# Optimization experiments

Measured on AMD Instinct MI355X. Metric: run time of the kernel, lower is better.

Reference implementation:

```python
import jax, jax.numpy as jnp
import numpy as np

EPS = 1.55e-5  # tf.math.l2_normalize epsilon semantics: x / sqrt(max(sum(x^2), eps))


def _l2norm_tokens(t):
    # normalize over the token axis (-2), matching tf.math.l2_normalize(axis=-2)
    sq = jnp.sum(t * t, axis=-2, keepdims=True)
    return t * jax.lax.rsqrt(jnp.maximum(sq, EPS))


def setup_inputs() -> dict:
    key = jax.random.key(0)
    ks = jax.random.split(key, 4)
    B, H, W, C = 16, 64, 64, 512
    heads = 8
    return {
        "x": jax.random.normal(ks[0], (B, H, W, C), jnp.float32),
        "qkv_w": jax.random.normal(ks[1], (C, 3 * C), jnp.float32) * (C ** -0.5),
        "q_bias": jnp.zeros((C,), jnp.float32),
        "v_bias": jnp.zeros((C,), jnp.float32),
        "scale": jnp.ones((heads, 1, 1), jnp.float32),
        "proj_w": jax.random.normal(ks[2], (C, C), jnp.float32) * (C ** -0.5),
        "proj_b": jnp.zeros((C,), jnp.float32),
    }


def reference(x, qkv_w, q_bias, v_bias, scale, proj_w, proj_b):
    B, H, W, C = x.shape
    heads = scale.shape[0]
    d = C // heads
    N = H * W

    # 1x1 conv QKV (no conv bias) + concatenated [q_bias, 0, v_bias]
    qkv = jnp.einsum("bhwc,cf->bhwf", x, qkv_w)
    qkv = qkv + jnp.concatenate([q_bias, jnp.zeros_like(q_bias), v_bias])
    # [B, N, heads, 3, d] -> [B, heads, N, 3, d]
    qkv = qkv.reshape(B, N, heads, 3, d).transpose(0, 2, 1, 3, 4)
    q, k, v = qkv[..., 0, :], qkv[..., 1, :], qkv[..., 2, :]  # each [B, heads, N, d]

    q = _l2norm_tokens(q)
    k = _l2norm_tokens(k)

    # channel-attention: [B, heads, d, d]
    attn = jnp.einsum("bhnd,bhne->bhde", q * jnp.exp(scale), k)
    attn = jax.nn.softmax(attn, axis=-1)

    # matmul(attn, v^T) -> [B, heads, d, N]; perm [0,3,1,2] -> [B, N, heads, d]
    out = jnp.einsum("bhde,bhne->bhdn", attn, v)
    out = out.transpose(0, 3, 1, 2).reshape(B, H, W, C)

    # output 1x1 conv projection with bias
    return jnp.einsum("bhwc,cf->bhwf", out, proj_w) + proj_b
```

## Files before the change

kernel.cpp:

```cpp
#include <hip/hip_runtime.h>
#include <stdint.h>
#include <stddef.h>

#define BATCH  16
#define HEADS  8
#define NTOK   4096
#define CDIM   512
#define FDIM   1536

typedef short bf16x8 __attribute__((ext_vector_type(8)));
typedef float fx4    __attribute__((ext_vector_type(4)));

__device__ __forceinline__ uint16_t f2bf(float f) {
    uint32_t u = __float_as_uint(f);
    return (uint16_t)((u + 0x7FFFu + ((u >> 16) & 1u)) >> 16);
}
__device__ __forceinline__ float bf2f(uint16_t u) {
    return __uint_as_float(((uint32_t)u) << 16);
}
__device__ __forceinline__ void gload16(const uint16_t* g, uint16_t* l) {
    __builtin_amdgcn_global_load_lds(
        (const __attribute__((address_space(1))) uint32_t*)(g),
        (__attribute__((address_space(3))) uint32_t*)(l), 16, 0, 0);
}

__global__ void transpose_w_kernel(const float* __restrict__ qkv_w,
                                   const float* __restrict__ proj_w,
                                   uint16_t* __restrict__ Wt,
                                   uint16_t* __restrict__ Pt) {
    __shared__ uint16_t tile[32][33];
    int blk = blockIdx.x;
    const float* src; uint16_t* dst; int W, Hh, r0, c0;
    if (blk < 768) {
        int tr = blk / 48, tc = blk % 48;
        src = qkv_w; dst = Wt; W = 1536; Hh = 512; r0 = tr * 32; c0 = tc * 32;
    } else {
        blk -= 768;
        int tr = blk / 16, tc = blk % 16;
        src = proj_w; dst = Pt; W = 512; Hh = 512; r0 = tr * 32; c0 = tc * 32;
    }
    const int tx = threadIdx.x & 31, ty = threadIdx.x >> 5;
    #pragma unroll
    for (int j = 0; j < 4; j++)
        tile[ty + 8 * j][tx] = f2bf(src[(size_t)(r0 + ty + 8 * j) * W + c0 + tx]);
    __syncthreads();
    #pragma unroll
    for (int j = 0; j < 4; j++)
        dst[(size_t)(c0 + ty + 8 * j) * Hh + r0 + tx] = tile[tx][ty + 8 * j];
}

__global__ void prep_kernel(const float* __restrict__ X,
                            uint16_t* __restrict__ Xb,
                            float* __restrict__ Sqk) {
    const int tid = blockIdx.x * blockDim.x + threadIdx.x;
    const int stride = gridDim.x * blockDim.x;
    for (int i = tid; i < (1 << 22); i += stride) {
        const fx4* src = reinterpret_cast<const fx4*>(X + (size_t)i * 8);
        fx4 v0 = src[0], v1 = src[1];
        union { bf16x8 v; uint16_t u[8]; } pk;
        #pragma unroll
        for (int e = 0; e < 4; e++) { pk.u[e] = f2bf(v0[e]); pk.u[4 + e] = f2bf(v1[e]); }
        reinterpret_cast<bf16x8*>(Xb)[i] = pk.v;
    }
    for (int i = tid; i < 16384; i += stride) Sqk[i] = 0.0f;
}

__global__ __launch_bounds__(256) void gemm_qkv_kernel(
        const uint16_t* __restrict__ Xb, const uint16_t* __restrict__ Wt,
        const float* __restrict__ q_bias, const float* __restrict__ v_bias,
        uint16_t* __restrict__ QT, uint16_t* __restrict__ KT,
        uint16_t* __restrict__ VT,
        float* __restrict__ Sq, float* __restrict__ Sk) {
    __shared__ uint16_t ring[3][8192];
    const int bx = blockIdx.x;
    const int swz = (bx & 7) * 768 + (bx >> 3);
    const int tm = swz / 12, tn = swz % 12;
    const int gm = tm * 128, gn = tn * 128;
    const int b = gm >> 12, tok0 = gm & 4095;
    const int t = threadIdx.x, lane = t & 63, w = t >> 6;
    const int wm = w >> 1, wn = w & 1;
    const int l15 = lane & 15, lg = lane >> 4;
    fx4 acc[4][4] = {};
    const int srow = t >> 2;
    const int scol = (((t & 3) ^ (srow & 3)) << 3);
    const uint16_t* gA = Xb + (size_t)(gm + srow) * 512 + scol;
    const uint16_t* gB = Wt + (size_t)(gn + srow) * 512 + scol;
    auto stage = [&](int kt_) {
        const int s_ = kt_ % 3;
        const int k0_ = kt_ * 32;
        gload16(gA + k0_,                    &ring[s_][t * 8]);
        gload16(gA + (size_t)64 * 512 + k0_, &ring[s_][t * 8 + 2048]);
        gload16(gB + k0_,                    &ring[s_][4096 + t * 8]);
        gload16(gB + (size_t)64 * 512 + k0_, &ring[s_][4096 + t * 8 + 2048]);
    };
    stage(0); stage(1);
    #pragma unroll
    for (int kt = 0; kt < 16; ++kt) {
        if (kt < 15) asm volatile("s_waitcnt vmcnt(4) lgkmcnt(0)" ::: "memory");
        else         asm volatile("s_waitcnt vmcnt(0) lgkmcnt(0)" ::: "memory");
        __builtin_amdgcn_s_barrier();
        if (kt < 14) stage(kt + 2);
        const uint16_t* As = &ring[kt % 3][0];
        const uint16_t* Bs = &ring[kt % 3][4096];
        bf16x8 af[4], bfr[4];
        #pragma unroll
        for (int m = 0; m < 4; m++) {
            const int row = wm * 64 + m * 16 + l15;
            af[m] = *reinterpret_cast<const bf16x8*>(&As[row * 32 + ((lg ^ (row & 3)) << 3)]);
        }
        #pragma unroll
        for (int n = 0; n < 4; n++) {
            const int row = wn * 64 + n * 16 + l15;
            bfr[n] = *reinterpret_cast<const bf16x8*>(&Bs[row * 32 + ((lg ^ (row & 3)) << 3)]);
        }
        __builtin_amdgcn_s_setprio(1);
        #pragma unroll
        for (int m = 0; m < 4; m++)
            #pragma unroll
            for (int n = 0; n < 4; n++)
                acc[m][n] = __builtin_amdgcn_mfma_f32_16x16x32_bf16(
                    af[m], bfr[n], acc[m][n], 0, 0, 0);
        __builtin_amdgcn_s_setprio(0);
    }
    __syncthreads();
    const int u = (gn >> 6) + wn;
    const int type = u % 3;
    const int h = u / 3;
    const int bh = b * 8 + h;
    float biasn[4];
    #pragma unroll
    for (int n = 0; n < 4; n++) {
        const int col = gn + wn * 64 + n * 16 + l15;
        biasn[n] = (col < 512) ? q_bias[col]
                  : ((col < 1024) ? 0.0f : v_bias[col - 1024]);
    }
    if (type < 2) {
        uint16_t* T = (type == 0) ? QT : KT;
        #pragma unroll
        for (int n = 0; n < 4; n++) {
            const int d = n * 16 + l15;
            uint16_t* dst = T + ((size_t)bh * 64 + d) * 4096 + tok0 + wm * 64 + lg * 4;
            float ss = 0.f;
            #pragma unroll
            for (int m = 0; m < 4; m++) {
                union { uint16_t u4[4]; uint64_t q; } pk;
                #pragma unroll
                for (int r = 0; r < 4; r++) {
                    const float f = acc[m][n][r] + biasn[n];
                    pk.u4[r] = f2bf(f);
                    ss += f * f;
                }
                *reinterpret_cast<uint64_t*>(dst + m * 16) = pk.q;
            }
            ss += __shfl_xor(ss, 16, 64);
            ss += __shfl_xor(ss, 32, 64);
            if (lg == 0)
                atomicAdd((type == 0 ? Sq : Sk) + bh * 64 + d, ss);
        }
    } else {
        uint16_t* vs = &ring[0][0];
        #pragma unroll
        for (int n = 0; n < 4; n++) {
            const int lcol = n * 16 + l15;
            #pragma unroll
            for (int m = 0; m < 4; m++)
                #pragma unroll
                for (int r = 0; r < 4; r++) {
                    const int lrow = wm * 64 + m * 16 + lg * 4 + r;
                    vs[lrow * 64 + (lcol ^ ((lrow & 7) << 3))] =
                        f2bf(acc[m][n][r] + biasn[n]);
                }
        }
    }
    __syncthreads();
    {
        const int u0 = gn >> 6;
        const int uv = (u0 % 3 == 2) ? u0 : (((u0 + 1) % 3 == 2) ? (u0 + 1) : -1);
        if (uv >= 0) {
            const uint16_t* vs = &ring[0][0];
            const int hv = uv / 3;
            const int row = t >> 1, c0v = (t & 1) * 32;
            uint16_t* dst = VT + (size_t)(gm + row) * 512 + hv * 64 + c0v;
            #pragma unroll
            for (int cc = 0; cc < 4; cc++) {
                const int col = c0v + cc * 8;
                bf16x8 vv = *reinterpret_cast<const bf16x8*>(
                    &vs[row * 64 + (col ^ ((row & 7) << 3))]);
                *reinterpret_cast<bf16x8*>(dst + cc * 8) = vv;
            }
        }
    }
}

__global__ __launch_bounds__(256) void attn_qk_kernel(
        const uint16_t* __restrict__ QT, const uint16_t* __restrict__ KT,
        float* __restrict__ Gpart) {
    __shared__ uint16_t Qs[2][8192];
    __shared__ uint16_t Ks[2][8192];
    const int blk = blockIdx.x;
    const int bh = blk >> 2, quarter = blk & 3;
    const int t = threadIdx.x, lane = t & 63, w = t >> 6;
    const int l15 = lane & 15, lg = lane >> 4;
    const int wr = w >> 1, wc = w & 1;
    fx4 acc[2][2] = {};
    const uint16_t* qbase = QT + (size_t)bh * 64 * 4096;
    const uint16_t* kbase = KT + (size_t)bh * 64 * 4096;
    auto stage = [&](int it_) {
        const int tokt = quarter * 1024 + it_ * 128;
        uint16_t* qd = &Qs[it_ & 1][0];
        uint16_t* kd = &Ks[it_ & 1][0];
        #pragma unroll
        for (int j = 0; j < 4; j++) {
            const int li = j * 256 + t;
            const int row = li >> 4;
            const int src_off = (((li & 15) ^ (row & 7)) << 3);
            gload16(qbase + (size_t)row * 4096 + tokt + src_off, qd + li * 8);
            gload16(kbase + (size_t)row * 4096 + tokt + src_off, kd + li * 8);
        }
    };
    stage(0);
    for (int it = 0; it < 8; it++) {
        asm volatile("s_waitcnt vmcnt(0) lgkmcnt(0)" ::: "memory");
        __builtin_amdgcn_s_barrier();
        if (it < 7) stage(it + 1);
        const uint16_t* Qb = &Qs[it & 1][0];
        const uint16_t* Kb = &Ks[it & 1][0];
        #pragma unroll
        for (int ks = 0; ks < 4; ks++) {
            const int kof = ks * 32 + lg * 8;
            const int ra0 = wr * 32 + l15,      ra1 = wr * 32 + 16 + l15;
            const int rb0 = wc * 32 + l15,      rb1 = wc * 32 + 16 + l15;
            bf16x8 a0 = *reinterpret_cast<const bf16x8*>(&Qb[ra0 * 128 + (kof ^ ((ra0 & 7) << 3))]);
            bf16x8 a1 = *reinterpret_cast<const bf16x8*>(&Qb[ra1 * 128 + (kof ^ ((ra1 & 7) << 3))]);
            bf16x8 b0 = *reinterpret_cast<const bf16x8*>(&Kb[rb0 * 128 + (kof ^ ((rb0 & 7) << 3))]);
            bf16x8 b1 = *reinterpret_cast<const bf16x8*>(&Kb[rb1 * 128 + (kof ^ ((rb1 & 7) << 3))]);
            acc[0][0] = __builtin_amdgcn_mfma_f32_16x16x32_bf16(a0, b0, acc[0][0], 0, 0, 0);
            acc[0][1] = __builtin_amdgcn_mfma_f32_16x16x32_bf16(a0, b1, acc[0][1], 0, 0, 0);
            acc[1][0] = __builtin_amdgcn_mfma_f32_16x16x32_bf16(a1, b0, acc[1][0], 0, 0, 0);
            acc[1][1] = __builtin_amdgcn_mfma_f32_16x16x32_bf16(a1, b1, acc[1][1], 0, 0, 0);
        }
    }
    float* gp = Gpart + (size_t)quarter * 524288 + (size_t)bh * 4096;
    #pragma unroll
    for (int mi = 0; mi < 2; mi++)
        #pragma unroll
        for (int ni = 0; ni < 2; ni++)
            #pragma unroll
            for (int r = 0; r < 4; r++) {
                const int d = wr * 32 + mi * 16 + lg * 4 + r;
                const int e = wc * 32 + ni * 16 + l15;
                gp[d * 64 + e] = acc[mi][ni][r];
            }
}

__global__ void attn_finalize_kernel(const float* __restrict__ Gpart,
                                     const float* __restrict__ Sq,
                                     const float* __restrict__ Sk,
                                     const float* __restrict__ scale,
                                     uint16_t* __restrict__ attnb) {
    const int bh = blockIdx.x;
    const int h = bh & 7;
    const int t = threadIdx.x;
    const int e = t & 63, w = t >> 6;
    const float es = expf(scale[h]);
    const float rk = rsqrtf(fmaxf(Sk[bh * 64 + e], 1.55e-5f));
    const float* g0 = Gpart + (size_t)bh * 4096;
    for (int d = w; d < 64; d += 4) {
        const float rq = rsqrtf(fmaxf(Sq[bh * 64 + d], 1.55e-5f));
        float g = g0[d * 64 + e] + g0[524288 + d * 64 + e]
                + g0[1048576 + d * 64 + e] + g0[1572864 + d * 64 + e];
        float x = es * g * rq * rk;
        float m = x;
        #pragma unroll
        for (int off = 32; off; off >>= 1) m = fmaxf(m, __shfl_xor(m, off, 64));
        float p = expf(x - m);
        float s = p;
        #pragma unroll
        for (int off = 32; off; off >>= 1) s += __shfl_xor(s, off, 64);
        attnb[(size_t)bh * 4096 + d * 64 + e] = f2bf(p / s);
    }
}

__global__ __launch_bounds__(256) void pv_kernel(
        const uint16_t* __restrict__ VT, const uint16_t* __restrict__ attnb,
        uint16_t* __restrict__ out_t) {
    __shared__ uint16_t Vs[64 * 64];
    __shared__ uint16_t Os[64 * 64];
    const int blk = blockIdx.x;
    const int bh = blk >> 6, chunk = blk & 63;
    const int b = bh >> 3, h = bh & 7;
    const int n0 = chunk * 64;
    const int t = threadIdx.x, lane = t & 63, w = t >> 6;
    const int l15 = lane & 15, lg = lane >> 4;
    #pragma unroll
    for (int j = 0; j < 2; j++) {
        const int li = j * 256 + t;
        const int row = li >> 3;
        const int src_off = (((li & 7) ^ (row & 7)) << 3);
        gload16(VT + (size_t)(b * NTOK + n0 + row) * 512 + h * 64 + src_off, &Vs[li * 8]);
    }
    bf16x8 bfr[4][2];
    const uint16_t* ab = attnb + (size_t)bh * 4096;
    #pragma unroll
    for (int n = 0; n < 4; n++)
        #pragma unroll
        for (int ks = 0; ks < 2; ks++)
            bfr[n][ks] = *reinterpret_cast<const bf16x8*>(ab + (n * 16 + l15) * 64 + ks * 32 + lg * 8);
    __syncthreads();
    fx4 acc[4] = {};
    #pragma unroll
    for (int ks = 0; ks < 2; ks++) {
        const int row = w * 16 + l15;
        const int kof = ks * 32 + lg * 8;
        bf16x8 a = *reinterpret_cast<const bf16x8*>(&Vs[row * 64 + (kof ^ ((row & 7) << 3))]);
        #pragma unroll
        for (int n = 0; n < 4; n++)
            acc[n] = __builtin_amdgcn_mfma_f32_16x16x32_bf16(a, bfr[n][ks], acc[n], 0, 0, 0);
    }
    #pragma unroll
    for (int n = 0; n < 4; n++)
        #pragma unroll
        for (int r = 0; r < 4; r++) {
            const int row = w * 16 + lg * 4 + r;
            const int col = n * 16 + l15;
            Os[row * 64 + (col ^ ((row & 7) << 3))] = f2bf(acc[n][r]);
        }
    __syncthreads();
    {
        const int tr = t >> 2, c0 = (t & 3) * 16;
        uint16_t* orow = out_t + (size_t)(b * NTOK + n0 + tr) * CDIM + h * 64;
        #pragma unroll
        for (int cc2 = 0; cc2 < 2; cc2++) {
            const int c = c0 + cc2 * 8;
            const int chnk = (c >> 3) ^ (tr & 7);
            bf16x8 vv = *reinterpret_cast<const bf16x8*>(&Os[tr * 64 + (chnk << 3)]);
            *reinterpret_cast<bf16x8*>(orow + c) = vv;
        }
    }
}

__global__ __launch_bounds__(256) void gemm_proj_kernel(
        const uint16_t* __restrict__ At, const uint16_t* __restrict__ Pt,
        const float* __restrict__ proj_b, float* __restrict__ outp) {
    __shared__ uint16_t ring[3][8192];
    const int bx = blockIdx.x;
    const int swz = (bx & 7) * 256 + (bx >> 3);
    const int tn = swz & 3, tm = swz >> 2;
    const int gm = tm * 128, gn = tn * 128;
    const int t = threadIdx.x, lane = t & 63, w = t >> 6;
    const int wm = w >> 1, wn = w & 1;
    const int l15 = lane & 15, lg = lane >> 4;
    fx4 acc[4][4] = {};
    const int srow = t >> 2;
    const int scol = (((t & 3) ^ (srow & 3)) << 3);
    const uint16_t* gA = At + (size_t)(gm + srow) * 512 + scol;
    const uint16_t* gB = Pt + (size_t)(gn + srow) * 512 + scol;
    auto stage = [&](int kt_) {
        const int s_ = kt_ % 3;
        const int k0_ = kt_ * 32;
        gload16(gA + k0_,                    &ring[s_][t * 8]);
        gload16(gA + (size_t)64 * 512 + k0_, &ring[s_][t * 8 + 2048]);
        gload16(gB + k0_,                    &ring[s_][4096 + t * 8]);
        gload16(gB + (size_t)64 * 512 + k0_, &ring[s_][4096 + t * 8 + 2048]);
    };
    stage(0); stage(1);
    #pragma unroll
    for (int kt = 0; kt < 16; ++kt) {
        if (kt < 15) asm volatile("s_waitcnt vmcnt(4) lgkmcnt(0)" ::: "memory");
        else         asm volatile("s_waitcnt vmcnt(0) lgkmcnt(0)" ::: "memory");
        __builtin_amdgcn_s_barrier();
        if (kt < 14) stage(kt + 2);
        const uint16_t* As = &ring[kt % 3][0];
        const uint16_t* Bs = &ring[kt % 3][4096];
        bf16x8 af[4], bfr[4];
        #pragma unroll
        for (int m = 0; m < 4; m++) {
            const int row = wm * 64 + m * 16 + l15;
            af[m] = *reinterpret_cast<const bf16x8*>(&As[row * 32 + ((lg ^ (row & 3)) << 3)]);
        }
        #pragma unroll
        for (int n = 0; n < 4; n++) {
            const int row = wn * 64 + n * 16 + l15;
            bfr[n] = *reinterpret_cast<const bf16x8*>(&Bs[row * 32 + ((lg ^ (row & 3)) << 3)]);
        }
        __builtin_amdgcn_s_setprio(1);
        #pragma unroll
        for (int m = 0; m < 4; m++)
            #pragma unroll
            for (int n = 0; n < 4; n++)
                acc[m][n] = __builtin_amdgcn_mfma_f32_16x16x32_bf16(
                    af[m], bfr[n], acc[m][n], 0, 0, 0);
        __builtin_amdgcn_s_setprio(0);
    }
    #pragma unroll
    for (int m = 0; m < 4; m++) {
        #pragma unroll
        for (int n = 0; n < 4; n++) {
            const int col = gn + wn * 64 + n * 16 + l15;
            const float bias = proj_b[col];
            #pragma unroll
            for (int r = 0; r < 4; r++) {
                const int row = gm + wm * 64 + m * 16 + lg * 4 + r;
                outp[(size_t)row * CDIM + col] = acc[m][n][r] + bias;
            }
        }
    }
}

extern "C" void kernel_launch(void* const* d_in, const int* in_sizes, int n_in,
                              void* d_out, int out_size, void* d_ws, size_t ws_size,
                              hipStream_t stream) {
    (void)in_sizes; (void)n_in; (void)out_size; (void)ws_size;
    const float* x      = (const float*)d_in[0];
    const float* qkv_w  = (const float*)d_in[1];
    const float* q_bias = (const float*)d_in[2];
    const float* v_bias = (const float*)d_in[3];
    const float* scale  = (const float*)d_in[4];
    const float* proj_w = (const float*)d_in[5];
    const float* proj_b = (const float*)d_in[6];
    float* out = (float*)d_out;

    char* wsp = (char*)d_ws;
    uint16_t* Wt    = (uint16_t*)(wsp);
    uint16_t* Pt    = (uint16_t*)(wsp + 1572864);
    float*    Sq    = (float*)   (wsp + 2097152);
    float*    Sk    = (float*)   (wsp + 2129920);
    float*    Gpart = (float*)   (wsp + 2162688);
    uint16_t* attnb = (uint16_t*)(wsp + 10551296);
    uint16_t* QT    = (uint16_t*)(wsp + 11599872);
    uint16_t* KT    = (uint16_t*)(wsp + 78708736);
    uint16_t* VT    = (uint16_t*)(wsp + 145817600);
    uint16_t* Xb    = (uint16_t*)(wsp + 212926464);
    uint16_t* out_t = Xb;

    hipLaunchKernelGGL(transpose_w_kernel, dim3(1024), dim3(256), 0, stream,
                       qkv_w, proj_w, Wt, Pt);
    hipLaunchKernelGGL(prep_kernel, dim3(2048), dim3(256), 0, stream,
                       x, Xb, Sq);
    hipLaunchKernelGGL(gemm_qkv_kernel, dim3(6144), dim3(256), 0, stream,
                       Xb, Wt, q_bias, v_bias, QT, KT, VT, Sq, Sk);
    hipLaunchKernelGGL(attn_qk_kernel, dim3(512), dim3(256), 0, stream,
                       QT, KT, Gpart);
    hipLaunchKernelGGL(attn_finalize_kernel, dim3(128), dim3(256), 0, stream,
                       Gpart, Sq, Sk, scale, attnb);
    hipLaunchKernelGGL(pv_kernel, dim3(8192), dim3(256), 0, stream,
                       VT, attnb, out_t);
    hipLaunchKernelGGL(gemm_proj_kernel, dim3(2048), dim3(256), 0, stream,
                       out_t, Pt, proj_b, out);
}
```

Before: 531.2 us.

## Use 256x256 eight-wave GEMM tiles with quadrant-phased double-buffered pipeline

Both the QKV and output projection GEMMs move from 128x128 tiles with 4 waves and a 3-stage ring to 256x256 tiles with 8 waves. Each K step is 64 wide and split into four quadrant phases that interleave global-to-LDS loads with MFMA work. The goal is more data reuse per tile and better overlap of loads with MFMA. In exchange it uses far more LDS and registers and more barriers, and the QKV epilogue now has to handle up to two V slices per tile.

Result: no change. 540.2 us (+1.7%).

```diff
diff --git a/kernel.cpp b/kernel.cpp
--- a/kernel.cpp
+++ b/kernel.cpp
@@ -65,131 +65,224 @@
     for (int i = tid; i < 16384; i += stride) Sqk[i] = 0.0f;
 }
 
-__global__ __launch_bounds__(256) void gemm_qkv_kernel(
+#define QPHASE(BUF, MH, NH, STAGE) do {                                        \
+    bf16x8 afr[4][2], bfr2[2][2];                                              \
+    _Pragma("unroll") for (int mi = 0; mi < 4; ++mi)                           \
+      _Pragma("unroll") for (int ks = 0; ks < 2; ++ks) {                       \
+        const int ra = wm * 64 + mi * 16 + l15;                                \
+        const int ch = ks * 4 + lg;                                            \
+        afr[mi][ks] = *reinterpret_cast<const bf16x8*>(                        \
+            &Ab[BUF][MH][ra * 64 + ((ch ^ (ra & 7)) << 3)]);                   \
+      }                                                                        \
+    _Pragma("unroll") for (int ni = 0; ni < 2; ++ni)                           \
+      _Pragma("unroll") for (int ks = 0; ks < 2; ++ks) {                       \
+        const int rb = wn * 32 + ni * 16 + l15;                                \
+        const int ch = ks * 4 + lg;                                            \
+        bfr2[ni][ks] = *reinterpret_cast<const bf16x8*>(                       \
+            &Bb[BUF][NH][rb * 64 + ((ch ^ (rb & 7)) << 3)]);                   \
+      }                                                                        \
+    STAGE;                                                                     \
+    asm volatile("s_waitcnt vmcnt(8)" ::: "memory");                           \
+    __builtin_amdgcn_s_barrier();                                              \
+    __builtin_amdgcn_s_setprio(1);                                             \
+    _Pragma("unroll") for (int mi = 0; mi < 4; ++mi)                           \
+      _Pragma("unroll") for (int ni = 0; ni < 2; ++ni)                         \
+        _Pragma("unroll") for (int ks = 0; ks < 2; ++ks)                       \
+          acc[MH][mi][NH][ni] = __builtin_amdgcn_mfma_f32_16x16x32_bf16(       \
+              afr[mi][ks], bfr2[ni][ks], acc[MH][mi][NH][ni], 0, 0, 0);        \
+    __builtin_amdgcn_s_setprio(0);                                             \
+    __builtin_amdgcn_s_barrier();                                              \
+  } while (0)
+
+__global__ __launch_bounds__(512, 2) void gemm_qkv_kernel(
         const uint16_t* __restrict__ Xb, const uint16_t* __restrict__ Wt,
         const float* __restrict__ q_bias, const float* __restrict__ v_bias,
         uint16_t* __restrict__ QT, uint16_t* __restrict__ KT,
         uint16_t* __restrict__ VT,
         float* __restrict__ Sq, float* __restrict__ Sk) {
-    __shared__ uint16_t ring[3][8192];
+    __shared__ uint16_t Ab[2][2][8192];
+    __shared__ uint16_t Bb[2][2][8192];
     const int bx = blockIdx.x;
-    const int swz = (bx & 7) * 768 + (bx >> 3);
-    const int tm = swz / 12, tn = swz % 12;
-    const int gm = tm * 128, gn = tn * 128;
-    const int b = gm >> 12, tok0 = gm & 4095;
+    const int swz = (bx & 7) * 192 + (bx >> 3);
+    const int tm = swz / 6, tn = swz % 6;
+    const int gm = tm * 256, gn = tn * 256;
+    const int b = gm >> 12;
     const int t = threadIdx.x, lane = t & 63, w = t >> 6;
-    const int wm = w >> 1, wn = w & 1;
-    const int l15 = lane & 15, lg = lane >> 4;
-    fx4 acc[4][4] = {};
-    const int srow = t >> 2;
-    const int scol = (((t & 3) ^ (srow & 3)) << 3);
-    const uint16_t* gA = Xb + (size_t)(gm + srow) * 512 + scol;
-    const uint16_t* gB = Wt + (size_t)(gn + srow) * 512 + scol;
-    auto stage = [&](int kt_) {
-        const int s_ = kt_ % 3;
-        const int k0_ = kt_ * 32;
-        gload16(gA + k0_,                    &ring[s_][t * 8]);
-        gload16(gA + (size_t)64 * 512 + k0_, &ring[s_][t * 8 + 2048]);
-        gload16(gB + k0_,                    &ring[s_][4096 + t * 8]);
-        gload16(gB + (size_t)64 * 512 + k0_, &ring[s_][4096 + t * 8 + 2048]);
+    const int wm = w >> 2, wn = w & 3;
+    const int l15 = lane & 15, lg = (lane >> 4) & 3;
+    fx4 acc[2][4][2][2] = {};
+    const int rowA = t >> 3;
+    const int swA = ((t & 7) ^ (rowA & 7)) << 3;
+    const uint16_t* gAb = Xb + (size_t)(gm + rowA) * 512 + swA;
+    const uint16_t* gBb = Wt + (size_t)(gn + rowA) * 512 + swA;
+    auto stA = [&](int kt_, int half) {
+        const int bufi = kt_ & 1; const int kc = (kt_ & 7) * 64;
+        gload16(gAb + (size_t)(half * 128) * 512 + kc,       &Ab[bufi][half][t * 8]);
+        gload16(gAb + (size_t)(half * 128 + 64) * 512 + kc,  &Ab[bufi][half][4096 + t * 8]);
     };
-    stage(0); stage(1);
-    #pragma unroll
-    for (int kt = 0; kt < 16; ++kt) {
-        if (kt < 15) asm volatile("s_waitcnt vmcnt(4) lgkmcnt(0)" ::: "memory");
-        else         asm volatile("s_waitcnt vmcnt(0) lgkmcnt(0)" ::: "memory");
-        __builtin_amdgcn_s_barrier();
-        if (kt < 14) stage(kt + 2);
-        const uint16_t* As = &ring[kt % 3][0];
-        const uint16_t* Bs = &ring[kt % 3][4096];
-        bf16x8 af[4], bfr[4];
-        #pragma unroll
-        for (int m = 0; m < 4; m++) {
-            const int row = wm * 64 + m * 16 + l15;
-            af[m] = *reinterpret_cast<const bf16x8*>(&As[row * 32 + ((lg ^ (row & 3)) << 3)]);
-        }
-        #pragma unroll
-        for (int n = 0; n < 4; n++) {
-            const int row = wn * 64 + n * 16 + l15;
-            bfr[n] = *reinterpret_cast<const bf16x8*>(&Bs[row * 32 + ((lg ^ (row & 3)) << 3)]);
-        }
-        __builtin_amdgcn_s_setprio(1);
-        #pragma unroll
-        for (int m = 0; m < 4; m++)
-            #pragma unroll
-            for (int n = 0; n < 4; n++)
-                acc[m][n] = __builtin_amdgcn_mfma_f32_16x16x32_bf16(
-                    af[m], bfr[n], acc[m][n], 0, 0, 0);
-        __builtin_amdgcn_s_setprio(0);
-    }
-    __syncthreads();
-    const int u = (gn >> 6) + wn;
-    const int type = u % 3;
-    const int h = u / 3;
-    const int bh = b * 8 + h;
-    float biasn[4];
-    #pragma unroll
-    for (int n = 0; n < 4; n++) {
-        const int col = gn + wn * 64 + n * 16 + l15;
-        biasn[n] = (col < 512) ? q_bias[col]
-                  : ((col < 1024) ? 0.0f : v_bias[col - 1024]);
-    }
-    if (type < 2) {
-        uint16_t* T = (type == 0) ? QT : KT;
-        #pragma unroll
-        for (int n = 0; n < 4; n++) {
-            const int d = n * 16 + l15;
-            uint16_t* dst = T + ((size_t)bh * 64 + d) * 4096 + tok0 + wm * 64 + lg * 4;
+    auto stB = [&](int kt_, int half) {
+        const int bufi = kt_ & 1; const int kc = (kt_ & 7) * 64;
+        gload16(gBb + (size_t)(half * 128) * 512 + kc,       &Bb[bufi][half][t * 8]);
+        gload16(gBb + (size_t)(half * 128 + 64) * 512 + kc,  &Bb[bufi][half][4096 + t * 8]);
+    };
+    stA(0, 0); stB(0, 0); stB(0, 1); stA(0, 1); stA(1, 0); stB(1, 0);
+    asm volatile("s_waitcnt vmcnt(8)" ::: "memory");
+    __builtin_amdgcn_s_barrier();
+    #pragma unroll
+    for (int i = 0; i < 4; ++i) {
+        const int kt = 2 * i;
+        QPHASE(0, 0, 0, stB(kt + 1, 1));
+        QPHASE(0, 0, 1, stA(kt + 1, 1));
+        QPHASE(0, 1, 0, stA(kt + 2, 0));
+        QPHASE(0, 1, 1, stB(kt + 2, 0));
+        QPHASE(1, 0, 0, stB(kt + 2, 1));
+        QPHASE(1, 0, 1, stA(kt + 2, 1));
+        QPHASE(1, 1, 0, stA(kt + 3, 0));
+        QPHASE(1, 1, 1, stB(kt + 3, 0));
+    }
+    asm volatile("s_waitcnt vmcnt(0)" ::: "memory");
+    __syncthreads();
+    int slotOf0 = -1, slotOf1 = -1, slotOf2 = -1, slotOf3 = -1;
+    {
+        int nv = 0;
+        if ((tn * 4 + 0) % 3 == 2) slotOf0 = nv++;
+        if ((tn * 4 + 1) % 3 == 2) slotOf1 = nv++;
+        if ((tn * 4 + 2) % 3 == 2) slotOf2 = nv++;
+        if ((tn * 4 + 3) % 3 == 2) slotOf3 = nv++;
+    }
+    uint16_t* vs = &Ab[0][0][0];
+    #pragma unroll
+    for (int nh = 0; nh < 2; ++nh)
+      #pragma unroll
+      for (int ni = 0; ni < 2; ++ni) {
+        const int cglob = gn + nh * 128 + wn * 32 + ni * 16 + l15;
+        const float bias = (cglob < 512) ? q_bias[cglob]
+                          : ((cglob < 1024) ? 0.0f : v_bias[cglob - 1024]);
+        const int c2 = (wn * 32 + ni * 16) >> 6;
+        const int c = nh * 2 + c2;
+        const int slot = (c == 0) ? slotOf0 : (c == 1) ? slotOf1
+                        : (c == 2) ? slotOf2 : slotOf3;
+        const int u = tn * 4 + c;
+        const int type = u % 3, h = u / 3;
+        if (slot < 0) {
+            uint16_t* T = (type == 0) ? QT : KT;
+            const int d = (cglob & 63);
+            const int bh = b * 8 + h;
+            uint16_t* dst0 = T + ((size_t)bh * 64 + d) * 4096 + (gm & 4095);
             float ss = 0.f;
             #pragma unroll
-            for (int m = 0; m < 4; m++) {
+            for (int mh = 0; mh < 2; ++mh)
+              #pragma unroll
+              for (int mi = 0; mi < 4; ++mi) {
                 union { uint16_t u4[4]; uint64_t q; } pk;
                 #pragma unroll
-                for (int r = 0; r < 4; r++) {
-                    const float f = acc[m][n][r] + biasn[n];
+                for (int r = 0; r < 4; ++r) {
+                    const float f = acc[mh][mi][nh][ni][r] + bias;
                     pk.u4[r] = f2bf(f);
                     ss += f * f;
                 }
-                *reinterpret_cast<uint64_t*>(dst + m * 16) = pk.q;
-            }
+                *reinterpret_cast<uint64_t*>(
+                    dst0 + mh * 128 + wm * 64 + mi * 16 + lg * 4) = pk.q;
+              }
             ss += __shfl_xor(ss, 16, 64);
             ss += __shfl_xor(ss, 32, 64);
             if (lg == 0)
                 atomicAdd((type == 0 ? Sq : Sk) + bh * 64 + d, ss);
-        }
-    } else {
-        uint16_t* vs = &ring[0][0];
-        #pragma unroll
-        for (int n = 0; n < 4; n++) {
-            const int lcol = n * 16 + l15;
+        } else {
+            const int lcol = (wn & 1) * 32 + ni * 16 + l15;
             #pragma unroll
-            for (int m = 0; m < 4; m++)
+            for (int mh = 0; mh < 2; ++mh)
+              #pragma unroll
+              for (int mi = 0; mi < 4; ++mi)
                 #pragma unroll
-                for (int r = 0; r < 4; r++) {
-                    const int lrow = wm * 64 + m * 16 + lg * 4 + r;
-                    vs[lrow * 64 + (lcol ^ ((lrow & 7) << 3))] =
-                        f2bf(acc[m][n][r] + biasn[n]);
+                for (int r = 0; r < 4; ++r) {
+                    const int row = mh * 128 + wm * 64 + mi * 16 + lg * 4 + r;
+                    vs[slot * 16384 + row * 64 +
+                       ((((lcol >> 3) ^ (row & 7)) << 3) | (lcol & 7))] =
+                        f2bf(acc[mh][mi][nh][ni][r] + bias);
                 }
         }
-    }
-    __syncthreads();
-    {
-        const int u0 = gn >> 6;
-        const int uv = (u0 % 3 == 2) ? u0 : (((u0 + 1) % 3 == 2) ? (u0 + 1) : -1);
-        if (uv >= 0) {
-            const uint16_t* vs = &ring[0][0];
-            const int hv = uv / 3;
+      }
+    __syncthreads();
+    #pragma unroll
+    for (int c = 0; c < 4; ++c) {
+        const int slot = (c == 0) ? slotOf0 : (c == 1) ? slotOf1
+                        : (c == 2) ? slotOf2 : slotOf3;
+        if (slot >= 0) {
+            const int hv = (tn * 4 + c) / 3;
             const int row = t >> 1, c0v = (t & 1) * 32;
             uint16_t* dst = VT + (size_t)(gm + row) * 512 + hv * 64 + c0v;
             #pragma unroll
-            for (int cc = 0; cc < 4; cc++) {
+            for (int cc = 0; cc < 4; ++cc) {
                 const int col = c0v + cc * 8;
                 bf16x8 vv = *reinterpret_cast<const bf16x8*>(
-                    &vs[row * 64 + (col ^ ((row & 7) << 3))]);
+                    &vs[slot * 16384 + row * 64 + (((col >> 3) ^ (row & 7)) << 3)]);
                 *reinterpret_cast<bf16x8*>(dst + cc * 8) = vv;
             }
         }
     }
+}
+
+__global__ __launch_bounds__(512, 2) void gemm_proj_kernel(
+        const uint16_t* __restrict__ At, const uint16_t* __restrict__ Pt,
+        const float* __restrict__ proj_b, float* __restrict__ outp) {
+    __shared__ uint16_t Ab[2][2][8192];
+    __shared__ uint16_t Bb[2][2][8192];
+    const int bx = blockIdx.x;
+    const int swz = (bx & 7) * 64 + (bx >> 3);
+    const int tm = swz >> 1, tn = swz & 1;
+    const int gm = tm * 256, gn = tn * 256;
+    const int t = threadIdx.x, lane = t & 63, w = t >> 6;
+    const int wm = w >> 2, wn = w & 3;
+    const int l15 = lane & 15, lg = (lane >> 4) & 3;
+    fx4 acc[2][4][2][2] = {};
+    const int rowA = t >> 3;
+    const int swA = ((t & 7) ^ (rowA & 7)) << 3;
+    const uint16_t* gAb = At + (size_t)(gm + rowA) * 512 + swA;
+    const uint16_t* gBb = Pt + (size_t)(gn + rowA) * 512 + swA;
+    auto stA = [&](int kt_, int half) {
+        const int bufi = kt_ & 1; const int kc = (kt_ & 7) * 64;
+        gload16(gAb + (size_t)(half * 128) * 512 + kc,      &Ab[bufi][half][t * 8]);
+        gload16(gAb + (size_t)(half * 128 + 64) * 512 + kc, &Ab[bufi][half][4096 + t * 8]);
+    };
+    auto stB = [&](int kt_, int half) {
+        const int bufi = kt_ & 1; const int kc = (kt_ & 7) * 64;
+        gload16(gBb + (size_t)(half * 128) * 512 + kc,      &Bb[bufi][half][t * 8]);
+        gload16(gBb + (size_t)(half * 128 + 64) * 512 + kc, &Bb[bufi][half][4096 + t * 8]);
+    };
+    stA(0, 0); stB(0, 0); stB(0, 1); stA(0, 1); stA(1, 0); stB(1, 0);
+    asm volatile("s_waitcnt vmcnt(8)" ::: "memory");
+    __builtin_amdgcn_s_barrier();
+    #pragma unroll
+    for (int i = 0; i < 4; ++i) {
+        const int kt = 2 * i;
+        QPHASE(0, 0, 0, stB(kt + 1, 1));
+        QPHASE(0, 0, 1, stA(kt + 1, 1));
+        QPHASE(0, 1, 0, stA(kt + 2, 0));
+        QPHASE(0, 1, 1, stB(kt + 2, 0));
+        QPHASE(1, 0, 0, stB(kt + 2, 1));
+        QPHASE(1, 0, 1, stA(kt + 2, 1));
+        QPHASE(1, 1, 0, stA(kt + 3, 0));
+        QPHASE(1, 1, 1, stB(kt + 3, 0));
+    }
+    asm volatile("s_waitcnt vmcnt(0)" ::: "memory");
+    __syncthreads();
+    #pragma unroll
+    for (int nh = 0; nh < 2; ++nh)
+      #pragma unroll
+      for (int ni = 0; ni < 2; ++ni) {
+        const int col = gn + nh * 128 + wn * 32 + ni * 16 + l15;
+        const float bias = proj_b[col];
+        #pragma unroll
+        for (int mh = 0; mh < 2; ++mh)
+          #pragma unroll
+          for (int mi = 0; mi < 4; ++mi)
+            #pragma unroll
+            for (int r = 0; r < 4; ++r) {
+                const int row = gm + mh * 128 + wm * 64 + mi * 16 + lg * 4 + r;
+                outp[(size_t)row * CDIM + col] = acc[mh][mi][nh][ni][r] + bias;
+            }
+      }
 }
 
 __global__ __launch_bounds__(256) void attn_qk_kernel(
@@ -339,74 +432,6 @@
     }
 }
 
-__global__ __launch_bounds__(256) void gemm_proj_kernel(
-        const uint16_t* __restrict__ At, const uint16_t* __restrict__ Pt,
-        const float* __restrict__ proj_b, float* __restrict__ outp) {
-    __shared__ uint16_t ring[3][8192];
-    const int bx = blockIdx.x;
-    const int swz = (bx & 7) * 256 + (bx >> 3);
-    const int tn = swz & 3, tm = swz >> 2;
-    const int gm = tm * 128, gn = tn * 128;
-    const int t = threadIdx.x, lane = t & 63, w = t >> 6;
-    const int wm = w >> 1, wn = w & 1;
-    const int l15 = lane & 15, lg = lane >> 4;
-    fx4 acc[4][4] = {};
-    const int srow = t >> 2;
-    const int scol = (((t & 3) ^ (srow & 3)) << 3);
-    const uint16_t* gA = At + (size_t)(gm + srow) * 512 + scol;
-    const uint16_t* gB = Pt + (size_t)(gn + srow) * 512 + scol;
-    auto stage = [&](int kt_) {
-        const int s_ = kt_ % 3;
-        const int k0_ = kt_ * 32;
-        gload16(gA + k0_,                    &ring[s_][t * 8]);
-        gload16(gA + (size_t)64 * 512 + k0_, &ring[s_][t * 8 + 2048]);
-        gload16(gB + k0_,                    &ring[s_][4096 + t * 8]);
-        gload16(gB + (size_t)64 * 512 + k0_, &ring[s_][4096 + t * 8 + 2048]);
-    };
-    stage(0); stage(1);
-    #pragma unroll
-    for (int kt = 0; kt < 16; ++kt) {
-        if (kt < 15) asm volatile("s_waitcnt vmcnt(4) lgkmcnt(0)" ::: "memory");
-        else         asm volatile("s_waitcnt vmcnt(0) lgkmcnt(0)" ::: "memory");
-        __builtin_amdgcn_s_barrier();
-        if (kt < 14) stage(kt + 2);
-        const uint16_t* As = &ring[kt % 3][0];
-        const uint16_t* Bs = &ring[kt % 3][4096];
-        bf16x8 af[4], bfr[4];
-        #pragma unroll
-        for (int m = 0; m < 4; m++) {
-            const int row = wm * 64 + m * 16 + l15;
-            af[m] = *reinterpret_cast<const bf16x8*>(&As[row * 32 + ((lg ^ (row & 3)) << 3)]);
-        }
-        #pragma unroll
-        for (int n = 0; n < 4; n++) {
-            const int row = wn * 64 + n * 16 + l15;
-            bfr[n] = *reinterpret_cast<const bf16x8*>(&Bs[row * 32 + ((lg ^ (row & 3)) << 3)]);
-        }
-        __builtin_amdgcn_s_setprio(1);
-        #pragma unroll
-        for (int m = 0; m < 4; m++)
-            #pragma unroll
-            for (int n = 0; n < 4; n++)
-                acc[m][n] = __builtin_amdgcn_mfma_f32_16x16x32_bf16(
-                    af[m], bfr[n], acc[m][n], 0, 0, 0);
-        __builtin_amdgcn_s_setprio(0);
-    }
-    #pragma unroll
-    for (int m = 0; m < 4; m++) {
-        #pragma unroll
-        for (int n = 0; n < 4; n++) {
-            const int col = gn + wn * 64 + n * 16 + l15;
-            const float bias = proj_b[col];
-            #pragma unroll
-            for (int r = 0; r < 4; r++) {
-                const int row = gm + wm * 64 + m * 16 + lg * 4 + r;
-                outp[(size_t)row * CDIM + col] = acc[m][n][r] + bias;
-            }
-        }
-    }
-}
-
 extern "C" void kernel_launch(void* const* d_in, const int* in_sizes, int n_in,
                               void* d_out, int out_size, void* d_ws, size_t ws_size,
                               hipStream_t stream) {
@@ -437,7 +462,7 @@
                        qkv_w, proj_w, Wt, Pt);
     hipLaunchKernelGGL(prep_kernel, dim3(2048), dim3(256), 0, stream,
                        x, Xb, Sq);
-    hipLaunchKernelGGL(gemm_qkv_kernel, dim3(6144), dim3(256), 0, stream,
+    hipLaunchKernelGGL(gemm_qkv_kernel, dim3(1536), dim3(512), 0, stream,
                        Xb, Wt, q_bias, v_bias, QT, KT, VT, Sq, Sk);
     hipLaunchKernelGGL(attn_qk_kernel, dim3(512), dim3(256), 0, stream,
                        QT, KT, Gpart);
@@ -445,6 +470,6 @@
                        Gpart, Sq, Sk, scale, attnb);
     hipLaunchKernelGGL(pv_kernel, dim3(8192), dim3(256), 0, stream,
                        VT, attnb, out_t);
-    hipLaunchKernelGGL(gemm_proj_kernel, dim3(2048), dim3(256), 0, stream,
+    hipLaunchKernelGGL(gemm_proj_kernel, dim3(512), dim3(512), 0, stream,
                        out_t, Pt, proj_b, out);
 }
```
